# Kernel optimization log

Hardware: AMD Instinct MI355X
Metric: run time of the kernel (lower is better)

Reference implementation:

```python
import jax, jax.numpy as jnp
import numpy as np

DIM = 1024
HEADS = 16
DIM_HEAD = 64
INNER = HEADS * DIM_HEAD  # 1024
SCALE = DIM_HEAD ** -0.5


def setup_inputs() -> dict:
    key = jax.random.key(0)
    ks = jax.random.split(key, 7)
    b, n = 4, 1024
    x = jax.random.normal(ks[0], (b, n, DIM), dtype=jnp.float32)
    # Dense kernels (glorot-ish scale), mix-head matrices are N(0,1) as in source
    Wq = jax.random.normal(ks[1], (DIM, INNER), dtype=jnp.float32) * (DIM ** -0.5)
    Wkv = jax.random.normal(ks[2], (DIM, 2 * INNER), dtype=jnp.float32) * (DIM ** -0.5)
    mix_pre = jax.random.normal(ks[3], (HEADS, HEADS), dtype=jnp.float32)
    mix_post = jax.random.normal(ks[4], (HEADS, HEADS), dtype=jnp.float32)
    Wo = jax.random.normal(ks[5], (INNER, DIM), dtype=jnp.float32) * (INNER ** -0.5)
    bo = jnp.zeros((DIM,), dtype=jnp.float32)
    return {"x": x, "Wq": Wq, "Wkv": Wkv, "mix_pre": mix_pre,
            "mix_post": mix_post, "Wo": Wo, "bo": bo}


def reference(x, Wq, Wkv, mix_pre, mix_post, Wo, bo):
    b, n, _ = x.shape
    # context = x (self-attention path)
    q = x @ Wq                      # [b, n, inner]
    kv = x @ Wkv                    # [b, n, 2*inner]
    k, v = jnp.split(kv, 2, axis=-1)
    split_heads = lambda t: t.reshape(b, n, HEADS, DIM_HEAD).transpose(0, 2, 1, 3)
    q, k, v = map(split_heads, (q, k, v))  # [b, h, n, d]
    dots = jnp.einsum('bhid,bhjd->bhij', q, k) * SCALE
    dots = jnp.einsum('bhij,hg->bgij', dots, mix_pre)   # talking-heads pre-softmax
    attn = jax.nn.softmax(dots, axis=-1)
    attn = jnp.einsum('bhij,hg->bgij', attn, mix_post)  # talking-heads post-softmax
    out = jnp.einsum('bhij,bhjd->bhid', attn, v)        # [b, h, n, d]
    out = out.transpose(0, 2, 1, 3).reshape(b, n, INNER)
    return out @ Wo + bo            # dropout rate 0 -> identity
```

## Files before the change

kernel.cpp:

```cpp
#include <hip/hip_runtime.h>
#include <hip/hip_bf16.h>

using bf16 = __hip_bfloat16;

typedef __bf16 bf16x8 __attribute__((ext_vector_type(8)));
typedef __bf16 bf16x2v __attribute__((ext_vector_type(2)));
typedef float  f32x4  __attribute__((ext_vector_type(4)));
typedef float  f32x2  __attribute__((ext_vector_type(2)));

#define QK_SCALE 0.125f

__device__ __forceinline__ void load_lds16(const bf16* g, bf16* l) {
  __builtin_amdgcn_global_load_lds(
      (const __attribute__((address_space(1))) unsigned int*)g,
      (__attribute__((address_space(3))) unsigned int*)l, 16, 0, 0);
}

__device__ __forceinline__ unsigned pack_bf2(float a, float b) {
  bf16x2v v;
  v[0] = (__bf16)a;
  v[1] = (__bf16)b;
  return __builtin_bit_cast(unsigned, v);
}

struct alignas(8) bf16x4s { bf16 a, b, c, d; };
__global__ void f32_to_bf16_k(const float4* __restrict__ in, bf16x4s* __restrict__ out, int n4)
{
  const int i = blockIdx.x * blockDim.x + threadIdx.x;
  if (i < n4) {
    const float4 v = in[i];
    out[i] = { (bf16)v.x, (bf16)v.y, (bf16)v.z, (bf16)v.w };
  }
}

template<int TM, int TN, int WM, int WN, bool BIAS, typename CT>
__global__ __launch_bounds__(256, 2)
void gemm_nt(const bf16* __restrict__ A, const bf16* __restrict__ B,
             CT* __restrict__ C, const float* __restrict__ bias,
             int K, int lda, int ldb, int ldc,
             long sA0, long sA1, long sB0, long sB1, long sC0, long sC1,
             int nz1, float alpha)
{
  constexpr int BK = 32;
  constexpr int LDE = TN + 8;
  constexpr unsigned SB_STAGE = (TM + TN) * BK * 2;
  constexpr unsigned SB_EP = (sizeof(CT) == 2) ? TM * LDE * 2 : 0;
  constexpr unsigned SBYTES = SB_STAGE > SB_EP ? SB_STAGE : SB_EP;
  __shared__ __align__(16) char smem[SBYTES];
  bf16* lsA = (bf16*)smem;
  bf16* lsB = lsA + TM * BK;

  const int z = blockIdx.z;
  A += (long)(z / nz1) * sA0 + (long)(z % nz1) * sA1;
  B += (long)(z / nz1) * sB0 + (long)(z % nz1) * sB1;
  C += (long)(z / nz1) * sC0 + (long)(z % nz1) * sC1;
  const int tm0 = blockIdx.y * TM;
  const int tn0 = blockIdx.x * TN;

  const int tid = threadIdx.x;
  const int w = tid >> 6, l = tid & 63;
  constexpr int WCOLS = TN / WN;
  const int wm = (w / WCOLS) * WM, wn = (w % WCOLS) * WN;
  constexpr int AM = WM / 16, AN = WN / 16;
  f32x4 acc[AM][AN] = {};
  const int kg = l >> 4, rl = l & 15;

  constexpr int RA = TM / 64, RB = TN / 64;
  const int srow0 = tid >> 2;
  const int scol = tid & 3;

  for (int k0 = 0; k0 < K; k0 += BK) {
#pragma unroll
    for (int r = 0; r < RA; ++r) {
      const int row = r * 64 + srow0;
      const int col8 = scol ^ ((row >> 1) & 3);
      load_lds16(A + (long)(tm0 + row) * lda + (k0 + col8 * 8),
                 &lsA[row * BK + scol * 8]);
    }
#pragma unroll
    for (int r = 0; r < RB; ++r) {
      const int row = r * 64 + srow0;
      const int col8 = scol ^ ((row >> 1) & 3);
      load_lds16(B + (long)(tn0 + row) * ldb + (k0 + col8 * 8),
                 &lsB[row * BK + scol * 8]);
    }
    __syncthreads();

    bf16x8 af[AM], bfr[AN];
#pragma unroll
    for (int i = 0; i < AM; ++i) {
      const int m = wm + i * 16 + rl;
      const int p = kg ^ ((m >> 1) & 3);
      af[i] = *(const bf16x8*)&lsA[m * BK + p * 8];
    }
#pragma unroll
    for (int j = 0; j < AN; ++j) {
      const int n = wn + j * 16 + rl;
      const int p = kg ^ ((n >> 1) & 3);
      bfr[j] = *(const bf16x8*)&lsB[n * BK + p * 8];
    }
#pragma unroll
    for (int i = 0; i < AM; ++i)
#pragma unroll
      for (int j = 0; j < AN; ++j)
        acc[i][j] = __builtin_amdgcn_mfma_f32_16x16x32_bf16(af[i], bfr[j], acc[i][j], 0, 0, 0);
    __syncthreads();
  }

  if constexpr (sizeof(CT) == 2) {
    bf16* ep = (bf16*)smem;
#pragma unroll
    for (int i = 0; i < AM; ++i) {
#pragma unroll
      for (int j = 0; j < AN; ++j) {
        const int col = wn + j * 16 + rl;
        float bv = 0.f;
        if (BIAS) bv = bias[tn0 + col];
#pragma unroll
        for (int v = 0; v < 4; ++v) {
          const int row = wm + i * 16 + (l >> 4) * 4 + v;
          ep[row * LDE + col] = (bf16)(acc[i][j][v] * alpha + bv);
        }
      }
    }
    __syncthreads();
    constexpr int CH = (TM * TN) / 2048;
#pragma unroll
    for (int c = 0; c < CH; ++c) {
      const int gidx = (c * 256 + tid) * 8;
      const int row = gidx / TN, col = gidx % TN;
      *(uint4*)&C[(long)(tm0 + row) * ldc + tn0 + col] = *(const uint4*)&ep[row * LDE + col];
    }
  } else {
#pragma unroll
    for (int i = 0; i < AM; ++i) {
#pragma unroll
      for (int j = 0; j < AN; ++j) {
        const int col = tn0 + wn + j * 16 + rl;
        float bv = 0.f;
        if (BIAS) bv = bias[col];
#pragma unroll
        for (int v = 0; v < 4; ++v) {
          const int row = tm0 + wm + i * 16 + (l >> 4) * 4 + v;
          C[(long)row * ldc + col] = (CT)(acc[i][j][v] * alpha + bv);
        }
      }
    }
  }
}

template<typename TI>
__global__ void transpose_k(const TI* __restrict__ in, bf16* __restrict__ out,
                            int ldi, int ldo,
                            long sI0, long sI1, long sO0, long sO1, int nz1)
{
  __shared__ bf16 t[32][33];
  const int z = blockIdx.z;
  in  += (long)(z / nz1) * sI0 + (long)(z % nz1) * sI1;
  out += (long)(z / nz1) * sO0 + (long)(z % nz1) * sO1;
  const int c0 = blockIdx.x * 32, r0 = blockIdx.y * 32;
  const int x = threadIdx.x, y = threadIdx.y;
#pragma unroll
  for (int dy = 0; dy < 32; dy += 8)
    t[y + dy][x] = (bf16)(float)in[(long)(r0 + y + dy) * ldi + c0 + x];
  __syncthreads();
#pragma unroll
  for (int dy = 0; dy < 32; dy += 8)
    out[(long)(c0 + y + dy) * ldo + r0 + x] = t[x][y + dy];
}

__global__ __launch_bounds__(256)
void mix_softmax_mix(bf16* __restrict__ S,
                     const float* __restrict__ mixpre, const float* __restrict__ mixpost)
{
  constexpr int LROW = 1032;
  __shared__ __align__(16) __bf16 lS[16 * LROW];
  __shared__ float pre[256], post[256];
  __shared__ float redZ[4][16];
  const int i = blockIdx.x, b = blockIdx.y;
  const int tid = threadIdx.x;
  pre[tid]  = mixpre[tid];
  post[tid] = mixpost[tid];
  const long hstr = 1048576L;
  bf16* Srow = S + (long)b * 16 * hstr + (long)i * 1024;
  const int w = tid >> 6, l = tid & 63;
  const int rl = l & 15, q = l >> 4;

#pragma unroll
  for (int r = 0; r < 8; ++r) {
    const int u = r * 256 + tid;
    const int h = u >> 7, jg = (u & 127) * 8;
    *(uint4*)&lS[h * LROW + jg] = *(const uint4*)&Srow[(long)h * hstr + jg];
  }
  __syncthreads();

  bf16x8 aHi, aLo;
#pragma unroll
  for (int e = 0; e < 8; ++e) {
    const int h = q * 8 + e;
    const float c = (h < 16) ? pre[(h & 15) * 16 + rl] : 0.f;
    const __bf16 hi = (__bf16)c;
    aHi[e] = hi;
    aLo[e] = (__bf16)(c - (float)hi);
  }

  const int hq = (q & 1) * 8;
  const int cw = w * 256;

  unsigned ph01[16], ph23[16];
  f32x4 zac = {0.f, 0.f, 0.f, 0.f};
#pragma unroll
  for (int c = 0; c < 16; ++c) {
    const int col = cw + c * 16 + rl;
    bf16x8 bfr;
#pragma unroll
    for (int e = 0; e < 8; ++e) bfr[e] = lS[(hq + e) * LROW + col];
    f32x4 d = __builtin_amdgcn_mfma_f32_16x16x32_bf16(aHi, bfr, f32x4{0.f,0.f,0.f,0.f}, 0, 0, 0);
    d = __builtin_amdgcn_mfma_f32_16x16x32_bf16(aLo, bfr, d, 0, 0, 0);
    float ev[4];
#pragma unroll
    for (int v = 0; v < 4; ++v) {
      ev[v] = __expf(d[v] - 10.f);
      zac[v] += ev[v];
    }
    ph01[c] = pack_bf2(ev[0], ev[1]);
    ph23[c] = pack_bf2(ev[2], ev[3]);
  }
#pragma unroll
  for (int off = 1; off < 16; off <<= 1) {
#pragma unroll
    for (int v = 0; v < 4; ++v) zac[v] += __shfl_xor(zac[v], off, 64);
  }
  if (rl == 0) {
#pragma unroll
    for (int v = 0; v < 4; ++v) redZ[w][q * 4 + v] = zac[v];
  }
  __syncthreads();

  bf16x8 pHi, pLo;
#pragma unroll
  for (int e = 0; e < 8; ++e) {
    const int g = q * 8 + e;
    float c = 0.f;
    if (g < 16) {
      const float Z = redZ[0][g & 15] + redZ[1][g & 15] + redZ[2][g & 15] + redZ[3][g & 15];
      c = post[(g & 15) * 16 + rl] / Z;
    }
    const __bf16 hi = (__bf16)c;
    pHi[e] = hi;
    pLo[e] = (__bf16)(c - (float)hi);
  }

  const int src0 = rl + 32 * (q & 1);
  const int src1 = src0 + 16;
#pragma unroll
  for (int c = 0; c < 16; ++c) {
    const unsigned d0 = (unsigned)__shfl((int)ph01[c], src0, 64);
    const unsigned d1 = (unsigned)__shfl((int)ph23[c], src0, 64);
    const unsigned d2 = (unsigned)__shfl((int)ph01[c], src1, 64);
    const unsigned d3 = (unsigned)__shfl((int)ph23[c], src1, 64);
    uint4 raw = {d0, d1, d2, d3};
    bf16x8 bfr = *(const bf16x8*)&raw;
    f32x4 d = __builtin_amdgcn_mfma_f32_16x16x32_bf16(pHi, bfr, f32x4{0.f,0.f,0.f,0.f}, 0, 0, 0);
    d = __builtin_amdgcn_mfma_f32_16x16x32_bf16(pLo, bfr, d, 0, 0, 0);
    const int col = cw + c * 16 + rl;
#pragma unroll
    for (int v = 0; v < 4; ++v)
      Srow[(long)(q * 4 + v) * hstr + col] = (bf16)d[v];
  }
}

extern "C" void kernel_launch(void* const* d_in, const int* in_sizes, int n_in,
                              void* d_out, int out_size, void* d_ws, size_t ws_size,
                              hipStream_t stream)
{
  const float* x     = (const float*)d_in[0];
  const float* Wq    = (const float*)d_in[1];
  const float* Wkv   = (const float*)d_in[2];
  const float* mpre  = (const float*)d_in[3];
  const float* mpost = (const float*)d_in[4];
  const float* Wo    = (const float*)d_in[5];
  const float* bo    = (const float*)d_in[6];
  float* out = (float*)d_out;

  char* ws = (char*)d_ws;
  const size_t MB = 1024 * 1024;
  if (ws_size < 184 * MB) return;
  bf16* xb   = (bf16*)(ws);
  bf16* QKV  = (bf16*)(ws + 8 * MB);
  bf16* WT   = (bf16*)(ws + 32 * MB);
  bf16* WoT  = (bf16*)(ws + 38 * MB);
  bf16* VT   = (bf16*)(ws + 40 * MB);
  bf16* Obuf = (bf16*)(ws + 48 * MB);
  bf16* Sbuf = (bf16*)(ws + 56 * MB);

  const dim3 tb(32, 8, 1);

  f32_to_bf16_k<<<4096, 256, 0, stream>>>((const float4*)x, (bf16x4s*)xb, 1048576);

  transpose_k<float><<<dim3(32, 32, 1), tb, 0, stream>>>(Wq,  WT,           1024, 1024, 0, 0, 0, 0, 1);
  transpose_k<float><<<dim3(64, 32, 1), tb, 0, stream>>>(Wkv, WT + 1048576, 2048, 1024, 0, 0, 0, 0, 1);
  transpose_k<float><<<dim3(32, 32, 1), tb, 0, stream>>>(Wo,  WoT,          1024, 1024, 0, 0, 0, 0, 1);

  gemm_nt<128, 128, 64, 64, false, bf16><<<dim3(24, 32, 1), 256, 0, stream>>>(
      xb, WT, QKV, nullptr, 1024, 1024, 1024, 3072, 0, 0, 0, 0, 0, 0, 1, 1.f);

  transpose_k<bf16><<<dim3(2, 32, 64), tb, 0, stream>>>(
      QKV + 2048, VT, 3072, 1024,
      3145728, 64, 16L * 65536, 65536, 16);

  gemm_nt<128, 128, 64, 64, false, bf16><<<dim3(8, 8, 64), 256, 0, stream>>>(
      QKV, QKV + 1024, Sbuf, nullptr, 64, 3072, 3072, 1024,
      3145728, 64, 3145728, 64, 16L * 1048576, 1048576, 16, QK_SCALE);

  mix_softmax_mix<<<dim3(1024, 4, 1), 256, 0, stream>>>(Sbuf, mpre, mpost);

  gemm_nt<64, 64, 32, 32, false, bf16><<<dim3(1, 16, 64), 256, 0, stream>>>(
      Sbuf, VT, Obuf, nullptr, 1024, 1024, 1024, 1024,
      16L * 1048576, 1048576, 16L * 65536, 65536, 1048576, 64, 16, 1.f);

  gemm_nt<128, 128, 64, 64, true, float><<<dim3(8, 32, 1), 256, 0, stream>>>(
      Obuf, WoT, out, bo, 1024, 1024, 1024, 1024, 0, 0, 0, 0, 0, 0, 1, 1.f);
}
```

Before: 269.6 us.

## Fuse talking-heads mix, softmax, post-mix and PV product into one kernel

Replaces the separate mix_softmax_mix kernel and the batched P·V GEMM with one kernel. Each 512-thread block handles 16 query rows of one batch across all heads. It streams the score tiles twice: one pass builds the softmax denominators and the second recomputes the exponentials, applies the post mix and multiplies by V. This removes the write-back and re-read of the full mixed attention matrix. The cost is recomputing the pre-mix and exponentials, using 32x32 MFMAs with hi/lo split rows, and launching only 256 blocks with one block per CU, which may limit occupancy. V is read directly from global memory without staging in LDS.

Result: slower. 311.5 us (+15.6%).

```diff
diff --git a/kernel.cpp b/kernel.cpp
--- a/kernel.cpp
+++ b/kernel.cpp
@@ -6,7 +6,7 @@
 typedef __bf16 bf16x8 __attribute__((ext_vector_type(8)));
 typedef __bf16 bf16x2v __attribute__((ext_vector_type(2)));
 typedef float  f32x4  __attribute__((ext_vector_type(4)));
-typedef float  f32x2  __attribute__((ext_vector_type(2)));
+typedef float  f32x16 __attribute__((ext_vector_type(16)));
 
 #define QK_SCALE 0.125f
 
@@ -169,104 +169,191 @@
     out[(long)(c0 + y + dy) * ldo + r0 + x] = t[x][y + dy];
 }
 
-__global__ __launch_bounds__(256)
-void mix_softmax_mix(bf16* __restrict__ S,
-                     const float* __restrict__ mixpre, const float* __restrict__ mixpost)
+#define LOADS(t)                                                               \
+  _Pragma("unroll")                                                            \
+  for (int it = 0; it < 4; ++it) {                                             \
+    const int u = it * 512 + tid;                                              \
+    const long off = (long)(u >> 8) * 2097152 + (long)((u >> 4) & 15) * 1024   \
+                   + (long)(t) * 64 + (u & 15) * 4;                            \
+    rA[it] = *(const uint2*)(Sb + off);                                        \
+    rB[it] = *(const uint2*)(Sb + off + 1048576);                              \
+  }
+
+#define STAGE()                                                                \
+  _Pragma("unroll")                                                            \
+  for (int it = 0; it < 4; ++it) {                                             \
+    const int u = it * 512 + tid;                                              \
+    uint4 wv;                                                                  \
+    wv.x = (rA[it].x & 0xFFFFu) | (rB[it].x << 16);                            \
+    wv.y = (rA[it].x >> 16)     | (rB[it].x & 0xFFFF0000u);                    \
+    wv.z = (rA[it].y & 0xFFFFu) | (rB[it].y << 16);                            \
+    wv.w = (rA[it].y >> 16)     | (rB[it].y & 0xFFFF0000u);                    \
+    *(uint4*)&SbL[(u >> 8) * 1088 + ((u >> 4) & 15) * 68 + (u & 15) * 4] = wv; \
+  }
+
+__global__ __launch_bounds__(512, 1)
+void mix_pv_fused(const bf16* __restrict__ S, const bf16* __restrict__ VTm,
+                  bf16* __restrict__ O,
+                  const float* __restrict__ mixpre, const float* __restrict__ mixpost)
 {
-  constexpr int LROW = 1032;
-  __shared__ __align__(16) __bf16 lS[16 * LROW];
-  __shared__ float pre[256], post[256];
-  __shared__ float redZ[4][16];
-  const int i = blockIdx.x, b = blockIdx.y;
+  __shared__ __align__(16) unsigned int SbL[8 * 16 * 68];
+  __shared__ __align__(16) __bf16 Pl[16 * 16 * 72];
+  __shared__ float preS[256], postS[256];
+
   const int tid = threadIdx.x;
-  pre[tid]  = mixpre[tid];
-  post[tid] = mixpost[tid];
-  const long hstr = 1048576L;
-  bf16* Srow = S + (long)b * 16 * hstr + (long)i * 1024;
-  const int w = tid >> 6, l = tid & 63;
-  const int rl = l & 15, q = l >> 4;
-
-#pragma unroll
-  for (int r = 0; r < 8; ++r) {
-    const int u = r * 256 + tid;
-    const int h = u >> 7, jg = (u & 127) * 8;
-    *(uint4*)&lS[h * LROW + jg] = *(const uint4*)&Srow[(long)h * hstr + jg];
-  }
+  const int l = tid & 63, w = tid >> 6;
+  const int bx = blockIdx.x;
+  const int b = bx & 3;
+  const int i0 = (bx >> 2) << 4;
+
+  if (tid < 256) preS[tid] = mixpre[tid];
+  else           postS[tid - 256] = mixpost[tid - 256];
   __syncthreads();
 
-  bf16x8 aHi, aLo;
+  const int col = l & 31;
+  const int H = l >> 5;
+  const int g16 = l & 15;
+  const bool loRow = (l & 16) != 0;
+
+  bf16x8 aPre, aPost;
 #pragma unroll
   for (int e = 0; e < 8; ++e) {
-    const int h = q * 8 + e;
-    const float c = (h < 16) ? pre[(h & 15) * 16 + rl] : 0.f;
-    const __bf16 hi = (__bf16)c;
-    aHi[e] = hi;
-    aLo[e] = (__bf16)(c - (float)hi);
-  }
-
-  const int hq = (q & 1) * 8;
-  const int cw = w * 256;
-
-  unsigned ph01[16], ph23[16];
-  f32x4 zac = {0.f, 0.f, 0.f, 0.f};
-#pragma unroll
-  for (int c = 0; c < 16; ++c) {
-    const int col = cw + c * 16 + rl;
-    bf16x8 bfr;
-#pragma unroll
-    for (int e = 0; e < 8; ++e) bfr[e] = lS[(hq + e) * LROW + col];
-    f32x4 d = __builtin_amdgcn_mfma_f32_16x16x32_bf16(aHi, bfr, f32x4{0.f,0.f,0.f,0.f}, 0, 0, 0);
-    d = __builtin_amdgcn_mfma_f32_16x16x32_bf16(aLo, bfr, d, 0, 0, 0);
-    float ev[4];
-#pragma unroll
-    for (int v = 0; v < 4; ++v) {
-      ev[v] = __expf(d[v] - 10.f);
-      zac[v] += ev[v];
-    }
-    ph01[c] = pack_bf2(ev[0], ev[1]);
-    ph23[c] = pack_bf2(ev[2], ev[3]);
-  }
-#pragma unroll
-  for (int off = 1; off < 16; off <<= 1) {
-#pragma unroll
-    for (int v = 0; v < 4; ++v) zac[v] += __shfl_xor(zac[v], off, 64);
-  }
-  if (rl == 0) {
-#pragma unroll
-    for (int v = 0; v < 4; ++v) redZ[w][q * 4 + v] = zac[v];
-  }
-  __syncthreads();
-
-  bf16x8 pHi, pLo;
-#pragma unroll
-  for (int e = 0; e < 8; ++e) {
-    const int g = q * 8 + e;
-    float c = 0.f;
-    if (g < 16) {
-      const float Z = redZ[0][g & 15] + redZ[1][g & 15] + redZ[2][g & 15] + redZ[3][g & 15];
-      c = post[(g & 15) * 16 + rl] / Z;
-    }
-    const __bf16 hi = (__bf16)c;
-    pHi[e] = hi;
-    pLo[e] = (__bf16)(c - (float)hi);
-  }
-
-  const int src0 = rl + 32 * (q & 1);
-  const int src1 = src0 + 16;
-#pragma unroll
-  for (int c = 0; c < 16; ++c) {
-    const unsigned d0 = (unsigned)__shfl((int)ph01[c], src0, 64);
-    const unsigned d1 = (unsigned)__shfl((int)ph23[c], src0, 64);
-    const unsigned d2 = (unsigned)__shfl((int)ph01[c], src1, 64);
-    const unsigned d3 = (unsigned)__shfl((int)ph23[c], src1, 64);
-    uint4 raw = {d0, d1, d2, d3};
-    bf16x8 bfr = *(const bf16x8*)&raw;
-    f32x4 d = __builtin_amdgcn_mfma_f32_16x16x32_bf16(pHi, bfr, f32x4{0.f,0.f,0.f,0.f}, 0, 0, 0);
-    d = __builtin_amdgcn_mfma_f32_16x16x32_bf16(pLo, bfr, d, 0, 0, 0);
-    const int col = cw + c * 16 + rl;
-#pragma unroll
-    for (int v = 0; v < 4; ++v)
-      Srow[(long)(q * 4 + v) * hstr + col] = (bf16)d[v];
+    const int k = H * 8 + e;
+    {
+      const float c = preS[k * 16 + g16];
+      const __bf16 hi = (__bf16)c;
+      aPre[e] = loRow ? (__bf16)(c - (float)hi) : hi;
+    }
+    {
+      const float c = postS[k * 16 + g16];
+      const __bf16 hi = (__bf16)c;
+      aPost[e] = loRow ? (__bf16)(c - (float)hi) : hi;
+    }
+  }
+
+  const bf16* Sb = S + (long)b * 16777216 + (long)i0 * 1024;
+
+  uint2 rA[4], rB[4];
+  float zac[2][8];
+#pragma unroll
+  for (int il = 0; il < 2; ++il)
+#pragma unroll
+    for (int k = 0; k < 8; ++k) zac[il][k] = 0.f;
+
+  LOADS(0)
+  for (int t = 0; t < 16; ++t) {
+    STAGE()
+    __syncthreads();
+    if (t < 15) { LOADS(t + 1) }
+#pragma unroll
+    for (int il = 0; il < 2; ++il) {
+      const int ic = 2 * w + il;
+#pragma unroll
+      for (int jh = 0; jh < 2; ++jh) {
+        const int base = H * 4352 + ic * 68 + jh * 32 + col;
+        uint4 bw;
+        bw.x = SbL[base];
+        bw.y = SbL[base + 1088];
+        bw.z = SbL[base + 2176];
+        bw.w = SbL[base + 3264];
+        const bf16x8 bfr = __builtin_bit_cast(bf16x8, bw);
+        f32x16 d = {};
+        d = __builtin_amdgcn_mfma_f32_32x32x16_bf16(aPre, bfr, d, 0, 0, 0);
+#pragma unroll
+        for (int k = 0; k < 8; ++k)
+          zac[il][k] += __expf(d[k] + d[k + 8] - 10.f);
+      }
+    }
+    __syncthreads();
+  }
+
+#pragma unroll
+  for (int il = 0; il < 2; ++il)
+#pragma unroll
+    for (int k = 0; k < 8; ++k) {
+      float z = zac[il][k];
+      z += __shfl_xor(z, 1, 64);
+      z += __shfl_xor(z, 2, 64);
+      z += __shfl_xor(z, 4, 64);
+      z += __shfl_xor(z, 8, 64);
+      z += __shfl_xor(z, 16, 64);
+      zac[il][k] = 1.f / z;
+    }
+
+  f32x4 acc[2][4] = {};
+  LOADS(0)
+  for (int t = 0; t < 16; ++t) {
+    STAGE()
+    __syncthreads();
+    if (t < 15) { LOADS(t + 1) }
+#pragma unroll
+    for (int il = 0; il < 2; ++il) {
+      const int ic = 2 * w + il;
+#pragma unroll
+      for (int jh = 0; jh < 2; ++jh) {
+        const int base = H * 4352 + ic * 68 + jh * 32 + col;
+        uint4 bw;
+        bw.x = SbL[base];
+        bw.y = SbL[base + 1088];
+        bw.z = SbL[base + 2176];
+        bw.w = SbL[base + 3264];
+        const bf16x8 bfr = __builtin_bit_cast(bf16x8, bw);
+        f32x16 d = {};
+        d = __builtin_amdgcn_mfma_f32_32x32x16_bf16(aPre, bfr, d, 0, 0, 0);
+        float pn[8];
+#pragma unroll
+        for (int k = 0; k < 8; ++k)
+          pn[k] = __expf(d[k] + d[k + 8] - 10.f) * zac[il][k];
+        const unsigned pA = pack_bf2(pn[0], pn[1]);
+        const unsigned pB = pack_bf2(pn[2], pn[3]);
+        const unsigned pC = pack_bf2(pn[4], pn[5]);
+        const unsigned pD = pack_bf2(pn[6], pn[7]);
+        const unsigned x0 = (unsigned)__shfl_xor((int)(H ? pA : pC), 32, 64);
+        const unsigned x1 = (unsigned)__shfl_xor((int)(H ? pB : pD), 32, 64);
+        uint4 praw;
+        praw.x = H ? x0 : pA;
+        praw.y = H ? x1 : pB;
+        praw.z = H ? pC : x0;
+        praw.w = H ? pD : x1;
+        const bf16x8 pfr = __builtin_bit_cast(bf16x8, praw);
+        f32x16 d2 = {};
+        d2 = __builtin_amdgcn_mfma_f32_32x32x16_bf16(aPost, pfr, d2, 0, 0, 0);
+#pragma unroll
+        for (int k = 0; k < 8; ++k) {
+          const int G = k + (k & 4) + (H << 2);
+          Pl[G * 1152 + ic * 72 + jh * 32 + col] = (__bf16)(d2[k] + d2[k + 8]);
+        }
+      }
+    }
+    __syncthreads();
+    const int jt = t * 64;
+#pragma unroll
+    for (int gi = 0; gi < 2; ++gi) {
+      const int G = w + gi * 8;
+      const bf16* vtg = VTm + ((long)(b * 16 + G) * 64) * 1024;
+#pragma unroll
+      for (int kc = 0; kc < 2; ++kc) {
+        const bf16x8 af = *(const bf16x8*)&Pl[G * 1152 + (l & 15) * 72 + kc * 32 + (l >> 4) * 8];
+#pragma unroll
+        for (int dt = 0; dt < 4; ++dt) {
+          const bf16x8 bfv = *(const bf16x8*)&vtg[(long)(dt * 16 + (l & 15)) * 1024
+                                                 + jt + kc * 32 + (l >> 4) * 8];
+          acc[gi][dt] = __builtin_amdgcn_mfma_f32_16x16x32_bf16(af, bfv, acc[gi][dt], 0, 0, 0);
+        }
+      }
+    }
+  }
+
+  const long ob = (long)(b * 1024 + i0) * 1024;
+#pragma unroll
+  for (int gi = 0; gi < 2; ++gi) {
+    const int G = w + gi * 8;
+#pragma unroll
+    for (int dt = 0; dt < 4; ++dt)
+#pragma unroll
+      for (int v = 0; v < 4; ++v)
+        O[ob + (long)((l >> 4) * 4 + v) * 1024 + G * 64 + dt * 16 + (l & 15)] =
+            (bf16)acc[gi][dt][v];
   }
 }
 
@@ -313,11 +400,7 @@
       QKV, QKV + 1024, Sbuf, nullptr, 64, 3072, 3072, 1024,
       3145728, 64, 3145728, 64, 16L * 1048576, 1048576, 16, QK_SCALE);
 
-  mix_softmax_mix<<<dim3(1024, 4, 1), 256, 0, stream>>>(Sbuf, mpre, mpost);
-
-  gemm_nt<64, 64, 32, 32, false, bf16><<<dim3(1, 16, 64), 256, 0, stream>>>(
-      Sbuf, VT, Obuf, nullptr, 1024, 1024, 1024, 1024,
-      16L * 1048576, 1048576, 16L * 65536, 65536, 1048576, 64, 16, 1.f);
+  mix_pv_fused<<<dim3(256, 1, 1), 512, 0, stream>>>(Sbuf, VT, Obuf, mpre, mpost);
 
   gemm_nt<128, 128, 64, 64, true, float><<<dim3(8, 32, 1), 256, 0, stream>>>(
       Obuf, WoT, out, bo, 1024, 1024, 1024, 1024, 0, 0, 0, 0, 0, 0, 1, 1.f);
```
